# Performance work log

Hardware: AMD Instinct MI355X
Metric: run time of the kernel (lower is better)

The kernel has to match this reference:

```python
import jax, jax.numpy as jnp
import numpy as np

NHEAD = 16


def setup_inputs() -> dict:
    key = jax.random.key(0)
    ks = jax.random.split(key, 6)
    S, B, D = 2048, 2, 1024
    std = float(np.sqrt(6.0 / (D + D)))  # xavier_uniform bound
    inp = {
        "query": jax.random.normal(ks[0], (S, B, D), jnp.float32),
        "key": jax.random.normal(ks[1], (S, B, D), jnp.float32),
        "value": jax.random.normal(ks[2], (S, B, D), jnp.float32),
        "Wq": jax.random.uniform(ks[3], (D, D), jnp.float32, -std, std),
        "bq": jnp.ones((D,), jnp.float32),
        "Wk": jax.random.uniform(ks[4], (D, D), jnp.float32, -std, std),
        "bk": jnp.ones((D,), jnp.float32),
        "Wv": jax.random.uniform(ks[5], (D, D), jnp.float32, -std, std),
        "bv": jnp.ones((D,), jnp.float32),
    }
    return inp


def reference(query, key, value, Wq, bq, Wk, bk, Wv, bv):
    S, B, D = query.shape
    h = NHEAD
    d = D // h
    scale = jnp.asarray(d ** 0.5, query.dtype)
    # projections (nn.Linear: x @ W^T + b)
    q = (query @ Wq.T + bq).reshape(S, B, h, d)
    k = (key @ Wk.T + bk).reshape(S, B, h, d)
    v = (value @ Wv.T + bv).reshape(S, B, h, d)
    # batch_first=False path: scores [b,h,i,j], softmax over j, then AV
    scores = jnp.einsum('ibhd,jbhd->bhij', q, k) / scale
    attn = jax.nn.softmax(scores, axis=-1)
    out = jnp.einsum('bhij,jbhd->ibhd', attn, v).reshape(S, B, D)
    return out
```

## Files before the change

### kernel.cpp

```cpp
#include <hip/hip_runtime.h>
#include <hip/hip_bf16.h>

#define S_LEN 2048
#define BATCH 2
#define DMODEL 1024
#define NHEAD 16
#define HDIM 64
#define MTOT (S_LEN * BATCH)
#define QKV_ELEMS ((size_t)MTOT * DMODEL)

typedef __bf16 bf16x8 __attribute__((ext_vector_type(8)));
typedef unsigned short u16x8 __attribute__((ext_vector_type(8)));
typedef float f32x4 __attribute__((ext_vector_type(4)));
typedef unsigned int u32x4 __attribute__((ext_vector_type(4)));

__device__ __forceinline__ unsigned short f2bf(float f) {
    unsigned int u = __float_as_uint(f);
    u += 0x7FFFu + ((u >> 16) & 1u);
    return (unsigned short)(u >> 16);
}

__device__ __forceinline__ unsigned int pack2(float lo, float hi) {
    __hip_bfloat162 h = __float22bfloat162_rn(make_float2(lo, hi));
    unsigned int r;
    __builtin_memcpy(&r, &h, 4);
    return r;
}

__device__ __forceinline__ void gload_lds16(const void* g, void* l) {
    __builtin_amdgcn_global_load_lds(
        (const __attribute__((address_space(1))) unsigned int*)g,
        (__attribute__((address_space(3))) unsigned int*)l, 16, 0, 0);
}

#define PBM 128
#define PBN 128
#define PBK 32
#define PLDS 48
#define QSCALE 0.18033688011112042f

__global__ __launch_bounds__(256) void proj_kernel(
        const float* __restrict__ Xq, const float* __restrict__ Xk,
        const float* __restrict__ Xv, const float* __restrict__ Wq,
        const float* __restrict__ Wk, const float* __restrict__ Wv,
        const float* __restrict__ bq, const float* __restrict__ bk,
        const float* __restrict__ bv, unsigned short* __restrict__ ws)
{
    const int work = (blockIdx.x & 7) * 96 + (blockIdx.x >> 3);
    const int t    = work >> 8;
    const int rem  = work & 255;
    const int m0   = (rem >> 3) * PBM;
    const int n0   = (rem & 7) * PBN;

    const float* X    = (t == 0) ? Xq : (t == 1) ? Xk : Xv;
    const float* W    = (t == 0) ? Wq : (t == 1) ? Wk : Wv;
    const float* bias = (t == 0) ? bq : (t == 1) ? bk : bv;
    unsigned short* out = ws + (size_t)t * QKV_ELEMS;
    const float scale = (t == 0) ? QSCALE : 1.0f;

    __shared__ __align__(16) unsigned short lds[(PBM + PBN) * PLDS];
    unsigned short* Alds = lds;
    unsigned short* Blds = lds + PBM * PLDS;

    const int tid = threadIdx.x;
    const int wave = tid >> 6;
    const int lane = tid & 63;
    const int lrow = lane & 15;
    const int lg   = lane >> 4;
    const int wr = (wave >> 1) * 64;
    const int wc = (wave & 1) * 64;

    f32x4 acc[4][4];
#pragma unroll
    for (int i = 0; i < 4; ++i)
#pragma unroll
        for (int j = 0; j < 4; ++j)
            acc[i][j] = (f32x4){0.f, 0.f, 0.f, 0.f};

    const int sr = tid >> 3;
    const int sg = tid & 7;

    for (int k0 = 0; k0 < DMODEL; k0 += PBK) {
        __syncthreads();
#pragma unroll
        for (int it = 0; it < 4; ++it) {
            const int row = sr + it * 32;
            const float4 va = *(const float4*)(X + (size_t)(m0 + row) * DMODEL + k0 + sg * 4);
            const float4 vb = *(const float4*)(W + (size_t)(n0 + row) * DMODEL + k0 + sg * 4);
            ushort4 ha, hb;
            ha.x = f2bf(va.x); ha.y = f2bf(va.y); ha.z = f2bf(va.z); ha.w = f2bf(va.w);
            hb.x = f2bf(vb.x); hb.y = f2bf(vb.y); hb.z = f2bf(vb.z); hb.w = f2bf(vb.w);
            *(ushort4*)&Alds[row * PLDS + sg * 4] = ha;
            *(ushort4*)&Blds[row * PLDS + sg * 4] = hb;
        }
        __syncthreads();

        bf16x8 af[4], bw[4];
#pragma unroll
        for (int i = 0; i < 4; ++i) {
            af[i] = *(const bf16x8*)&Alds[(wr + i * 16 + lrow) * PLDS + lg * 8];
            bw[i] = *(const bf16x8*)&Blds[(wc + i * 16 + lrow) * PLDS + lg * 8];
        }
#pragma unroll
        for (int i = 0; i < 4; ++i)
#pragma unroll
            for (int j = 0; j < 4; ++j)
                acc[i][j] = __builtin_amdgcn_mfma_f32_16x16x32_bf16(af[i], bw[j], acc[i][j], 0, 0, 0);
    }

#pragma unroll
    for (int j = 0; j < 4; ++j) {
        const int n  = n0 + wc + j * 16 + lrow;
        const float bv_ = bias[n];
        const int h  = n >> 6;
        const int dd = n & 63;
#pragma unroll
        for (int i = 0; i < 4; ++i) {
#pragma unroll
            for (int r = 0; r < 4; ++r) {
                const int m = m0 + wr + i * 16 + lg * 4 + r;
                const int s = m >> 1;
                const int b = m & 1;
                const float v = (acc[i][j][r] + bv_) * scale;
                size_t idx;
                if (t == 2)
                    idx = ((size_t)((b * NHEAD + h) * HDIM + dd)) * S_LEN + s;
                else
                    idx = ((size_t)((b * NHEAD + h) * S_LEN + s)) * HDIM + dd;
                out[idx] = f2bf(v);
            }
        }
    }
}

#define NT (S_LEN / 64)
#define PUSTR 17

__global__ __launch_bounds__(512, 4) void attn_kernel(
        const unsigned short* __restrict__ ws, float* __restrict__ out)
{
    const unsigned short* Qw = ws;
    const unsigned short* Kw = ws + QKV_ELEMS;
    const unsigned short* Vw = ws + 2 * QKV_ELEMS;

    const int bid = blockIdx.x;
    const int idx = bid >> 3;
    const int bh  = (bid & 7) * 4 + (idx >> 4);
    const int q0  = (idx & 15) * 128;

    __shared__ __align__(16) unsigned short Kbuf[2][64 * 64];
    __shared__ __align__(16) unsigned short Vbuf[2][64 * 64];
    __shared__ unsigned int Pu[8][32 * PUSTR];

    const int tid  = threadIdx.x;
    const int wave = tid >> 6;
    const int lane = tid & 63;
    const int lrow = lane & 15;
    const int lg   = lane >> 4;

    const size_t base = (size_t)bh * S_LEN * HDIM;
    const int qrow = q0 + wave * 16 + lrow;

    bf16x8 qf[2];
#pragma unroll
    for (int c = 0; c < 2; ++c)
        qf[c] = *(const bf16x8*)(Qw + base + (size_t)qrow * HDIM + c * 32 + lg * 8);

    bf16x8 ones;
    {
        u16x8 o;
#pragma unroll
        for (int e = 0; e < 8; ++e) o[e] = 0x3F80;
        ones = __builtin_bit_cast(bf16x8, o);
    }

    f32x4 O[4], Lacc;
#pragma unroll
    for (int dt = 0; dt < 4; ++dt) O[dt] = (f32x4){0.f, 0.f, 0.f, 0.f};
    Lacc = (f32x4){0.f, 0.f, 0.f, 0.f};
    float mrun = -__builtin_inff();

    const int srow = tid >> 3;
    const int sgrp = (tid & 7) ^ (srow & 7);
    const int dsto = tid * 8;

    gload_lds16(Kw + base + (size_t)srow * HDIM + sgrp * 8,  &Kbuf[0][dsto]);
    gload_lds16(Vw + base + (size_t)srow * S_LEN + sgrp * 8, &Vbuf[0][dsto]);
    __syncthreads();

    int cur = 0;
    for (int t = 0; t < NT; ++t) {
        if (t + 1 < NT) {
            const int sn = (t + 1) * 64;
            gload_lds16(Kw + base + (size_t)(sn + srow) * HDIM + sgrp * 8, &Kbuf[cur ^ 1][dsto]);
            gload_lds16(Vw + base + (size_t)srow * S_LEN + sn + sgrp * 8, &Vbuf[cur ^ 1][dsto]);
        }

        const unsigned short* Klds = Kbuf[cur];
        const unsigned short* Vlds = Vbuf[cur];

        f32x4 S[4];
#pragma unroll
        for (int kt = 0; kt < 4; ++kt) S[kt] = (f32x4){0.f, 0.f, 0.f, 0.f};
        __builtin_amdgcn_s_setprio(1);
#pragma unroll
        for (int kt = 0; kt < 4; ++kt) {
#pragma unroll
            for (int c = 0; c < 2; ++c) {
                const int g = ((c * 4 + lg) ^ (lrow & 7)) * 8;
                const bf16x8 ka = *(const bf16x8*)&Klds[(kt * 16 + lrow) * 64 + g];
                S[kt] = __builtin_amdgcn_mfma_f32_16x16x32_bf16(ka, qf[c], S[kt], 0, 0, 0);
            }
        }
        __builtin_amdgcn_s_setprio(0);

        float m0_ = fmaxf(fmaxf(S[0][0], S[0][1]), fmaxf(S[0][2], S[0][3]));
        float m1_ = fmaxf(fmaxf(S[1][0], S[1][1]), fmaxf(S[1][2], S[1][3]));
        float m2_ = fmaxf(fmaxf(S[2][0], S[2][1]), fmaxf(S[2][2], S[2][3]));
        float m3_ = fmaxf(fmaxf(S[3][0], S[3][1]), fmaxf(S[3][2], S[3][3]));
        float mx = fmaxf(fmaxf(m0_, m1_), fmaxf(m2_, m3_));
        mx = fmaxf(mx, __shfl_xor(mx, 16, 64));
        mx = fmaxf(mx, __shfl_xor(mx, 32, 64));

        if (!__all(mx - mrun <= 8.0f)) {
            const float mnew = fmaxf(mrun, mx);
            const float ex   = exp2f(mrun - mnew);
            mrun = mnew;
#pragma unroll
            for (int dt = 0; dt < 4; ++dt) O[dt] *= ex;
            Lacc *= ex;
        }

#pragma unroll
        for (int kt = 0; kt < 4; ++kt)
#pragma unroll
            for (int r = 0; r < 4; ++r)
                S[kt][r] = exp2f(S[kt][r] - mrun);

#pragma unroll
        for (int kt = 0; kt < 4; ++kt) {
#pragma unroll
            for (int i = 0; i < 2; ++i) {
                const unsigned int dw = pack2(S[kt][2 * i], S[kt][2 * i + 1]);
                const int kp = kt * 8 + lg * 2 + i;
                Pu[wave][kp * PUSTR + lrow] = dw;
            }
        }
        __asm__ volatile("" ::: "memory");

        __builtin_amdgcn_s_setprio(1);
        bf16x8 pb[2];
#pragma unroll
        for (int c = 0; c < 2; ++c) {
            u32x4 pu;
#pragma unroll
            for (int e = 0; e < 4; ++e)
                pu[e] = Pu[wave][(c * 16 + lg * 4 + e) * PUSTR + lrow];
            pb[c] = __builtin_bit_cast(bf16x8, pu);
        }
#pragma unroll
        for (int dt = 0; dt < 4; ++dt) {
#pragma unroll
            for (int c = 0; c < 2; ++c) {
                const int g = ((c * 4 + lg) ^ (lrow & 7)) * 8;
                const bf16x8 va = *(const bf16x8*)&Vlds[(dt * 16 + lrow) * 64 + g];
                O[dt] = __builtin_amdgcn_mfma_f32_16x16x32_bf16(va, pb[c], O[dt], 0, 0, 0);
            }
        }
        Lacc = __builtin_amdgcn_mfma_f32_16x16x32_bf16(ones, pb[0], Lacc, 0, 0, 0);
        Lacc = __builtin_amdgcn_mfma_f32_16x16x32_bf16(ones, pb[1], Lacc, 0, 0, 0);
        __builtin_amdgcn_s_setprio(0);

        __syncthreads();
        cur ^= 1;
    }

    const int bb = bh >> 4;
    const int hh = bh & 15;
    const float inv = 1.0f / Lacc[0];
    float* op = out + (size_t)qrow * (BATCH * DMODEL) + bb * DMODEL + hh * HDIM;
#pragma unroll
    for (int dt = 0; dt < 4; ++dt) {
        float4 v;
        v.x = O[dt][0] * inv; v.y = O[dt][1] * inv;
        v.z = O[dt][2] * inv; v.w = O[dt][3] * inv;
        *(float4*)(op + dt * 16 + lg * 4) = v;
    }
}

extern "C" void kernel_launch(void* const* d_in, const int* in_sizes, int n_in,
                              void* d_out, int out_size, void* d_ws, size_t ws_size,
                              hipStream_t stream) {
    const float* q  = (const float*)d_in[0];
    const float* k  = (const float*)d_in[1];
    const float* v  = (const float*)d_in[2];
    const float* Wq = (const float*)d_in[3];
    const float* bq = (const float*)d_in[4];
    const float* Wk = (const float*)d_in[5];
    const float* bk = (const float*)d_in[6];
    const float* Wv = (const float*)d_in[7];
    const float* bv = (const float*)d_in[8];
    unsigned short* ws = (unsigned short*)d_ws;
    float* out = (float*)d_out;

    proj_kernel<<<dim3(768), dim3(256), 0, stream>>>(q, k, v, Wq, Wk, Wv, bq, bk, bv, ws);
    attn_kernel<<<dim3(512), dim3(512), 0, stream>>>(ws, out);
}
```

Before: 143.4 us.

## Pre-convert inputs to bf16 and double-buffer projection GEMM via direct LDS loads

```diff
diff --git a/kernel.cpp b/kernel.cpp
--- a/kernel.cpp
+++ b/kernel.cpp
@@ -8,6 +8,9 @@
 #define HDIM 64
 #define MTOT (S_LEN * BATCH)
 #define QKV_ELEMS ((size_t)MTOT * DMODEL)
+#define XOFF (3 * QKV_ELEMS)
+#define WOFF (XOFF + 3 * QKV_ELEMS)
+#define WSEG ((size_t)DMODEL * DMODEL)
 
 typedef __bf16 bf16x8 __attribute__((ext_vector_type(8)));
 typedef unsigned short u16x8 __attribute__((ext_vector_type(8)));
@@ -33,18 +36,45 @@
         (__attribute__((address_space(3))) unsigned int*)l, 16, 0, 0);
 }
 
+__global__ __launch_bounds__(256) void cvt_kernel(
+        const float* __restrict__ Xq, const float* __restrict__ Xk,
+        const float* __restrict__ Xv, const float* __restrict__ Wq,
+        const float* __restrict__ Wk, const float* __restrict__ Wv,
+        unsigned short* __restrict__ ws)
+{
+    const int seg = blockIdx.y;
+    const float* src;
+    unsigned short* dst;
+    int n4;
+    if (seg < 3) {
+        src = (seg == 0) ? Xq : (seg == 1) ? Xk : Xv;
+        dst = ws + XOFF + (size_t)seg * QKV_ELEMS;
+        n4  = (int)(QKV_ELEMS / 4);
+    } else {
+        const int s = seg - 3;
+        src = (s == 0) ? Wq : (s == 1) ? Wk : Wv;
+        dst = ws + WOFF + (size_t)s * WSEG;
+        n4  = (int)(WSEG / 4);
+    }
+    const int stride = gridDim.x * blockDim.x;
+    for (int i = blockIdx.x * blockDim.x + threadIdx.x; i < n4; i += stride) {
+        const float4 v = ((const float4*)src)[i];
+        uint2 o;
+        o.x = pack2(v.x, v.y);
+        o.y = pack2(v.z, v.w);
+        ((uint2*)dst)[i] = o;
+    }
+}
+
 #define PBM 128
 #define PBN 128
 #define PBK 32
-#define PLDS 48
 #define QSCALE 0.18033688011112042f
 
-__global__ __launch_bounds__(256) void proj_kernel(
-        const float* __restrict__ Xq, const float* __restrict__ Xk,
-        const float* __restrict__ Xv, const float* __restrict__ Wq,
-        const float* __restrict__ Wk, const float* __restrict__ Wv,
+__global__ __launch_bounds__(256, 3) void proj_kernel(
+        const unsigned short* __restrict__ wsin,
         const float* __restrict__ bq, const float* __restrict__ bk,
-        const float* __restrict__ bv, unsigned short* __restrict__ ws)
+        const float* __restrict__ bv, unsigned short* __restrict__ wsout)
 {
     const int work = (blockIdx.x & 7) * 96 + (blockIdx.x >> 3);
     const int t    = work >> 8;
@@ -52,17 +82,16 @@
     const int m0   = (rem >> 3) * PBM;
     const int n0   = (rem & 7) * PBN;
 
-    const float* X    = (t == 0) ? Xq : (t == 1) ? Xk : Xv;
-    const float* W    = (t == 0) ? Wq : (t == 1) ? Wk : Wv;
+    const unsigned short* X = wsin + XOFF + (size_t)t * QKV_ELEMS;
+    const unsigned short* W = wsin + WOFF + (size_t)t * WSEG;
     const float* bias = (t == 0) ? bq : (t == 1) ? bk : bv;
-    unsigned short* out = ws + (size_t)t * QKV_ELEMS;
+    unsigned short* out = wsout + (size_t)t * QKV_ELEMS;
     const float scale = (t == 0) ? QSCALE : 1.0f;
 
-    __shared__ __align__(16) unsigned short lds[(PBM + PBN) * PLDS];
-    unsigned short* Alds = lds;
-    unsigned short* Blds = lds + PBM * PLDS;
-
-    const int tid = threadIdx.x;
+    __shared__ __align__(16) unsigned short Abuf[2][PBM * PBK];
+    __shared__ __align__(16) unsigned short Bbuf[2][PBN * PBK];
+
+    const int tid  = threadIdx.x;
     const int wave = tid >> 6;
     const int lane = tid & 63;
     const int lrow = lane & 15;
@@ -77,35 +106,49 @@
         for (int j = 0; j < 4; ++j)
             acc[i][j] = (f32x4){0.f, 0.f, 0.f, 0.f};
 
-    const int sr = tid >> 3;
-    const int sg = tid & 7;
-
+    const int srow_ = tid >> 2;
+    const int sc_   = tid & 3;
+    const int gsw = (lg ^ (lrow & 3)) * 8;
+
+#pragma unroll
+    for (int i0 = 0; i0 < 2; ++i0) {
+        const int row = i0 * 64 + srow_;
+        const int c   = sc_ ^ (row & 3);
+        gload_lds16(X + (size_t)(m0 + row) * DMODEL + c * 8, &Abuf[0][i0 * 2048 + tid * 8]);
+        gload_lds16(W + (size_t)(n0 + row) * DMODEL + c * 8, &Bbuf[0][i0 * 2048 + tid * 8]);
+    }
+    __syncthreads();
+
+    int cur = 0;
     for (int k0 = 0; k0 < DMODEL; k0 += PBK) {
-        __syncthreads();
-#pragma unroll
-        for (int it = 0; it < 4; ++it) {
-            const int row = sr + it * 32;
-            const float4 va = *(const float4*)(X + (size_t)(m0 + row) * DMODEL + k0 + sg * 4);
-            const float4 vb = *(const float4*)(W + (size_t)(n0 + row) * DMODEL + k0 + sg * 4);
-            ushort4 ha, hb;
-            ha.x = f2bf(va.x); ha.y = f2bf(va.y); ha.z = f2bf(va.z); ha.w = f2bf(va.w);
-            hb.x = f2bf(vb.x); hb.y = f2bf(vb.y); hb.z = f2bf(vb.z); hb.w = f2bf(vb.w);
-            *(ushort4*)&Alds[row * PLDS + sg * 4] = ha;
-            *(ushort4*)&Blds[row * PLDS + sg * 4] = hb;
-        }
-        __syncthreads();
+        if (k0 + PBK < DMODEL) {
+#pragma unroll
+            for (int i0 = 0; i0 < 2; ++i0) {
+                const int row = i0 * 64 + srow_;
+                const int c   = sc_ ^ (row & 3);
+                gload_lds16(X + (size_t)(m0 + row) * DMODEL + k0 + PBK + c * 8,
+                            &Abuf[cur ^ 1][i0 * 2048 + tid * 8]);
+                gload_lds16(W + (size_t)(n0 + row) * DMODEL + k0 + PBK + c * 8,
+                            &Bbuf[cur ^ 1][i0 * 2048 + tid * 8]);
+            }
+        }
 
         bf16x8 af[4], bw[4];
 #pragma unroll
         for (int i = 0; i < 4; ++i) {
-            af[i] = *(const bf16x8*)&Alds[(wr + i * 16 + lrow) * PLDS + lg * 8];
-            bw[i] = *(const bf16x8*)&Blds[(wc + i * 16 + lrow) * PLDS + lg * 8];
-        }
+            af[i] = *(const bf16x8*)&Abuf[cur][(wr + i * 16 + lrow) * PBK + gsw];
+            bw[i] = *(const bf16x8*)&Bbuf[cur][(wc + i * 16 + lrow) * PBK + gsw];
+        }
+        __builtin_amdgcn_s_setprio(1);
 #pragma unroll
         for (int i = 0; i < 4; ++i)
 #pragma unroll
             for (int j = 0; j < 4; ++j)
                 acc[i][j] = __builtin_amdgcn_mfma_f32_16x16x32_bf16(af[i], bw[j], acc[i][j], 0, 0, 0);
+        __builtin_amdgcn_s_setprio(0);
+
+        __syncthreads();
+        cur ^= 1;
     }
 
 #pragma unroll
@@ -303,6 +346,7 @@
     unsigned short* ws = (unsigned short*)d_ws;
     float* out = (float*)d_out;
 
-    proj_kernel<<<dim3(768), dim3(256), 0, stream>>>(q, k, v, Wq, Wk, Wv, bq, bk, bv, ws);
+    cvt_kernel<<<dim3(1024, 6), dim3(256), 0, stream>>>(q, k, v, Wq, Wk, Wv, ws);
+    proj_kernel<<<dim3(768), dim3(256), 0, stream>>>(ws, bq, bk, bv, ws);
     attn_kernel<<<dim3(512), dim3(512), 0, stream>>>(ws, out);
 }
```

Result: faster. 138.1 us (-3.7%).
